# Kernel tuning notes

Measured on AMD Instinct MI355X. Metric: run time of the kernel, lower is better.

Reference implementation:

```python
import jax, jax.numpy as jnp
import numpy as np

IN_FEATURES = 512
HIDDEN_DIM = 512
B, S = 8, 2048


def setup_inputs() -> dict:
    key = jax.random.key(0)
    ks = jax.random.split(key, 7)
    sc_in = 1.0 / np.sqrt(IN_FEATURES)
    return {
        "x": jax.random.normal(ks[0], (B, S, IN_FEATURES), dtype=jnp.float32),
        "Wq": jax.random.normal(ks[1], (IN_FEATURES, HIDDEN_DIM), dtype=jnp.float32) * sc_in,
        "bq": jax.random.normal(ks[2], (HIDDEN_DIM,), dtype=jnp.float32) * 0.01,
        "Wk": jax.random.normal(ks[3], (IN_FEATURES, HIDDEN_DIM), dtype=jnp.float32) * sc_in,
        "bk": jax.random.normal(ks[4], (HIDDEN_DIM,), dtype=jnp.float32) * 0.01,
        "Wv": jax.random.normal(ks[5], (IN_FEATURES, HIDDEN_DIM), dtype=jnp.float32) * sc_in,
        "bv": jax.random.normal(ks[6], (HIDDEN_DIM,), dtype=jnp.float32) * 0.01,
    }


def reference(x, Wq, bq, Wk, bk, Wv, bv):
    # x: [B, S, in_features]
    q = jnp.einsum("bsf,fh->bsh", x, Wq) + bq  # [B, S, H]
    k = jnp.einsum("bsf,fh->bsh", x, Wk) + bk
    v = jnp.einsum("bsf,fh->bsh", x, Wv) + bv
    scale = 1.0 / jnp.sqrt(jnp.asarray(q.shape[-1], dtype=q.dtype))
    scores = jnp.einsum("bqh,bkh->bqk", q, k) * scale  # [B, S, S]
    weights = jax.nn.softmax(scores, axis=-1)
    return jnp.einsum("bqk,bkh->bqh", weights, v)  # [B, S, H]
```

## Files before the change

### kernel.cpp

```cpp
#include <hip/hip_runtime.h>
#include <hip/hip_bf16.h>

typedef __bf16 bf16;
typedef __bf16 bf16x8 __attribute__((ext_vector_type(8)));
typedef float  f32x4  __attribute__((ext_vector_type(4)));

#define MFMA16(a,b,c) __builtin_amdgcn_mfma_f32_16x16x32_bf16((a),(b),(c),0,0,0)

static const int BATCH = 8;
static const int SEQ   = 2048;
static const int HID   = 512;
static const int MTOT  = BATCH * SEQ;

__device__ __forceinline__ void gl2lds16(const void* g, void* l) {
    __builtin_amdgcn_global_load_lds(
        (const __attribute__((address_space(1))) void*)g,
        (__attribute__((address_space(3))) void*)l, 16, 0, 0);
}

__global__ void k_convert_x(const float* __restrict__ x, bf16* __restrict__ xb, int n4) {
    int i = blockIdx.x * blockDim.x + threadIdx.x;
    int stride = gridDim.x * blockDim.x;
    for (; i < n4; i += stride) {
        float4 v = ((const float4*)x)[i];
        union { bf16 h[4]; uint2 u; } o;
        o.h[0] = (bf16)v.x; o.h[1] = (bf16)v.y; o.h[2] = (bf16)v.z; o.h[3] = (bf16)v.w;
        ((uint2*)xb)[i] = o.u;
    }
}

__global__ void k_transpose_w(const float* __restrict__ Wq, const float* __restrict__ Wk,
                              const float* __restrict__ Wv, bf16* __restrict__ wt) {
    int z = blockIdx.z;
    const float* W = (z == 0) ? Wq : (z == 1) ? Wk : Wv;
    bf16* WT = wt + (size_t)z * HID * HID;
    __shared__ float tile[32][33];
    int t  = threadIdx.x;
    int tx = t & 31, ty = t >> 5;
    int f0 = blockIdx.y * 32, h0 = blockIdx.x * 32;
    for (int i = 0; i < 32; i += 8)
        tile[ty + i][tx] = W[(size_t)(f0 + ty + i) * HID + h0 + tx];
    __syncthreads();
    for (int i = 0; i < 32; i += 8)
        WT[(size_t)(h0 + ty + i) * HID + f0 + tx] = (bf16)tile[tx][ty + i];
}

__global__ __launch_bounds__(256) void
k_qkv(const bf16* __restrict__ xb, const bf16* __restrict__ wt,
      const float* __restrict__ bq, const float* __restrict__ bk, const float* __restrict__ bv,
      bf16* __restrict__ qb, bf16* __restrict__ kb, bf16* __restrict__ vt) {
    __shared__ __align__(16) char sm[65536];
    int z = blockIdx.z;
    const bf16*  WT   = wt + (size_t)z * HID * HID;
    const float* bias = (z == 0) ? bq : (z == 1) ? bk : bv;
    float scale = (z == 0) ? 0.044194173824159216f : 1.0f;

    int m0 = blockIdx.y * 128, n0 = blockIdx.x * 128;
    int t = threadIdx.x;
    int w = t >> 6, lane = t & 63, quad = lane >> 4, l15 = lane & 15;
    int wr = w >> 1, wc = w & 1;

    int rowA = t >> 3;
    int chS  = (t & 7) ^ (rowA & 7);
    const char* xga = (const char*)xb + ((size_t)(m0 + rowA) * 512 + chS * 8) * 2;
    const char* wga = (const char*)WT + ((size_t)(n0 + rowA) * 512 + chS * 8) * 2;

    const char* aK0 = sm + (wr * 64 + l15) * 128 + ((quad ^ (l15 & 7)) * 16);
    const char* aK1 = sm + (wr * 64 + l15) * 128 + (((4 + quad) ^ (l15 & 7)) * 16);
    const char* bK0 = sm + 16384 + (wc * 64 + l15) * 128 + ((quad ^ (l15 & 7)) * 16);
    const char* bK1 = sm + 16384 + (wc * 64 + l15) * 128 + (((4 + quad) ^ (l15 & 7)) * 16);

    f32x4 acc[4][4] = {};

#define QSTAGE(S)                                                             \
    {                                                                         \
        _Pragma("unroll")                                                     \
        for (int i = 0; i < 4; i++)                                           \
            gl2lds16(xga + i * 32768, sm + (S) * 32768 + i * 4096 + w * 1024);\
        _Pragma("unroll")                                                     \
        for (int i = 0; i < 4; i++)                                           \
            gl2lds16(wga + i * 32768,                                         \
                     sm + (S) * 32768 + 16384 + i * 4096 + w * 1024);         \
        xga += 128; wga += 128;                                               \
    }

#define QCOMP(CUR)                                                            \
    {                                                                         \
        bf16x8 af[4], bfr[4];                                                 \
        _Pragma("unroll")                                                     \
        for (int mt = 0; mt < 4; mt++)                                        \
            af[mt] = *(const bf16x8*)(aK0 + mt * 2048 + (CUR) * 32768);       \
        _Pragma("unroll")                                                     \
        for (int nt = 0; nt < 4; nt++)                                        \
            bfr[nt] = *(const bf16x8*)(bK0 + nt * 2048 + (CUR) * 32768);      \
        _Pragma("unroll")                                                     \
        for (int mt = 0; mt < 4; mt++)                                        \
            _Pragma("unroll")                                                 \
            for (int nt = 0; nt < 4; nt++)                                    \
                acc[mt][nt] = MFMA16(af[mt], bfr[nt], acc[mt][nt]);           \
        _Pragma("unroll")                                                     \
        for (int mt = 0; mt < 4; mt++)                                        \
            af[mt] = *(const bf16x8*)(aK1 + mt * 2048 + (CUR) * 32768);       \
        _Pragma("unroll")                                                     \
        for (int nt = 0; nt < 4; nt++)                                        \
            bfr[nt] = *(const bf16x8*)(bK1 + nt * 2048 + (CUR) * 32768);      \
        _Pragma("unroll")                                                     \
        for (int mt = 0; mt < 4; mt++)                                        \
            _Pragma("unroll")                                                 \
            for (int nt = 0; nt < 4; nt++)                                    \
                acc[mt][nt] = MFMA16(af[mt], bfr[nt], acc[mt][nt]);           \
    }

    QSTAGE(0);
    __syncthreads();
    for (int ii = 0; ii < 4; ii++) {
        QSTAGE(1);
        QCOMP(0);
        __syncthreads();
        if (ii < 3) QSTAGE(0);
        QCOMP(1);
        __syncthreads();
    }
#undef QSTAGE
#undef QCOMP

    if (z < 2) {
        bf16* out = (z == 0) ? qb : kb;
#pragma unroll
        for (int nt = 0; nt < 4; nt++) {
            int col = n0 + wc * 64 + nt * 16 + l15;
            float bc = bias[col];
#pragma unroll
            for (int mt = 0; mt < 4; mt++) {
                int rowb = m0 + wr * 64 + mt * 16 + quad * 4;
#pragma unroll
                for (int r = 0; r < 4; r++) {
                    float v = (acc[mt][nt][r] + bc) * scale;
                    out[(size_t)(rowb + r) * HID + col] = (bf16)v;
                }
            }
        }
    } else {
        bf16* st = (bf16*)sm;
#pragma unroll
        for (int nt = 0; nt < 4; nt++) {
            int colL = wc * 64 + nt * 16 + l15;
            float bc = bias[n0 + colL];
#pragma unroll
            for (int mt = 0; mt < 4; mt++) {
                int rowL = wr * 64 + mt * 16 + quad * 4;
#pragma unroll
                for (int r = 0; r < 4; r++)
                    st[(size_t)colL * 136 + rowL + r] = (bf16)(acc[mt][nt][r] + bc);
            }
        }
        __syncthreads();
        int b  = m0 >> 11;
        int s0 = m0 & 2047;
        bf16* vbase = vt + ((size_t)b * HID + n0) * SEQ + s0;
#pragma unroll
        for (int i = 0; i < 8; i++) {
            int p = i * 256 + t;
            int colL = p >> 4, ch = p & 15;
            *(uint4*)((char*)vbase + (size_t)colL * SEQ * 2 + ch * 16) =
                *(const uint4*)&st[(size_t)colL * 136 + ch * 8];
        }
    }
}

__global__ __launch_bounds__(512, 2) void
k_attn(const bf16* __restrict__ qb, const bf16* __restrict__ kbuf,
       const bf16* __restrict__ vt, float* __restrict__ out) {
    __shared__ __align__(16) char smem[76288];
    char* sm = smem;

    int j = blockIdx.x;
    int b = j & 7, qblk = j >> 3;
    int t = threadIdx.x, w = t >> 6, lane = t & 63, quad = lane >> 4, l15 = lane & 15;
    int rg = w & 3, kg = w >> 2;

    const bf16* Qrow   = qb + ((size_t)b * SEQ + qblk * 64 + rg * 16) * HID;
    const bf16* Kbase  = kbuf + (size_t)b * SEQ * HID;
    const bf16* VTbase = vt + (size_t)b * HID * SEQ;

    const char* kE = sm + (kg * 16 + l15) * 1024 + ((quad ^ (l15 & 7)) * 16);
    const char* kO = sm + (kg * 16 + l15) * 1024 + (((4 + quad) ^ (l15 & 7)) * 16);
    char*       pW = sm + 65536 + (rg * 16 + quad * 4) * 80 + (kg * 16 + l15) * 2;
    const char* pR = sm + 65536 + l15 * 80 + quad * 16;
    float*      mlx = (float*)(sm + 75776);

    const char* kgp = (const char*)Kbase + w * 1024 + ((lane ^ w) * 16);
    const char* vgp = (const char*)VTbase + (size_t)(w * 64 + l15) * 4096 + quad * 16;

    bf16x8 qf[16];
#pragma unroll
    for (int kt = 0; kt < 16; kt++)
        qf[kt] = *(const bf16x8*)&Qrow[(size_t)l15 * HID + kt * 32 + quad * 8];

    float l_acc[4] = {0.f, 0.f, 0.f, 0.f};
    f32x4 o_acc[16] = {};
    bf16x8 vf[2][4];

    const int NIT = SEQ / 32;

#define STAGE(S)                                                              \
    {                                                                         \
        _Pragma("unroll")                                                     \
        for (int jj = 0; jj < 4; jj++)                                        \
            gl2lds16(kgp + jj * 8192,                                         \
                     sm + (S) * 32768 + jj * 8192 + w * 1024);                \
        kgp += 32768;                                                         \
        __builtin_amdgcn_sched_barrier(0);                                    \
    }

#define VLOAD(VP)                                                             \
    {                                                                         \
        _Pragma("unroll")                                                     \
        for (int hs = 0; hs < 4; hs++)                                        \
            vf[VP][hs] = *(const bf16x8*)(vgp + hs * 65536);                  \
        vgp += 64;                                                            \
    }

#define QKP(CUR)                                                              \
    {                                                                         \
        f32x4 sa = {}, sb = {};                                               \
        __builtin_amdgcn_s_setprio(1);                                        \
        _Pragma("unroll")                                                     \
        for (int kp = 0; kp < 8; kp++) {                                      \
            bf16x8 kfe = *(const bf16x8*)(kE + kp * 128 + (CUR) * 32768);     \
            bf16x8 kfo = *(const bf16x8*)(kO + kp * 128 + (CUR) * 32768);     \
            sa = MFMA16(qf[2 * kp], kfe, sa);                                 \
            sb = MFMA16(qf[2 * kp + 1], kfo, sb);                             \
        }                                                                     \
        __builtin_amdgcn_s_setprio(0);                                        \
        _Pragma("unroll")                                                     \
        for (int r = 0; r < 4; r++) {                                         \
            float p = __expf(sa[r] + sb[r] - 8.0f);                           \
            l_acc[r] += p;                                                    \
            *(bf16*)(pW + (CUR) * 5120 + r * 80) = (bf16)p;                   \
        }                                                                     \
    }

#define PV(PB, VP)                                                            \
    {                                                                         \
        bf16x8 pa0 = *(const bf16x8*)(pR + (PB) * 5120 + 0 * 1280);           \
        bf16x8 pa1 = *(const bf16x8*)(pR + (PB) * 5120 + 1 * 1280);           \
        bf16x8 pa2 = *(const bf16x8*)(pR + (PB) * 5120 + 2 * 1280);           \
        bf16x8 pa3 = *(const bf16x8*)(pR + (PB) * 5120 + 3 * 1280);           \
        __builtin_amdgcn_s_setprio(1);                                        \
        _Pragma("unroll")                                                     \
        for (int hs = 0; hs < 4; hs++) {                                      \
            o_acc[0 * 4 + hs] = MFMA16(pa0, vf[VP][hs], o_acc[0 * 4 + hs]);   \
            o_acc[1 * 4 + hs] = MFMA16(pa1, vf[VP][hs], o_acc[1 * 4 + hs]);   \
            o_acc[2 * 4 + hs] = MFMA16(pa2, vf[VP][hs], o_acc[2 * 4 + hs]);   \
            o_acc[3 * 4 + hs] = MFMA16(pa3, vf[VP][hs], o_acc[3 * 4 + hs]);   \
        }                                                                     \
        __builtin_amdgcn_s_setprio(0);                                        \
    }

#define BAR()                                                                 \
    {                                                                         \
        asm volatile("s_waitcnt vmcnt(0) lgkmcnt(0)" ::: "memory");           \
        __builtin_amdgcn_sched_barrier(0);                                    \
        __builtin_amdgcn_s_barrier();                                         \
        __builtin_amdgcn_sched_barrier(0);                                    \
    }

    STAGE(0);

    BAR();
    STAGE(1);
    VLOAD(0);
    QKP(0);

    BAR();
    STAGE(0);
    VLOAD(1);
    PV(0, 0);
    QKP(1);

    for (int ii = 1; ii < NIT / 2; ii++) {
        BAR();
        STAGE(1);
        VLOAD(0);
        PV(1, 1);
        QKP(0);
        BAR();
        if (ii < NIT / 2 - 1) STAGE(0);
        VLOAD(1);
        PV(0, 0);
        QKP(1);
    }

    BAR();
    PV(1, 1);

    float lw[4];
#pragma unroll
    for (int r = 0; r < 4; r++) {
        float v = l_acc[r];
        for (int d = 1; d < 16; d <<= 1) v += __shfl_xor(v, d, 64);
        lw[r] = v;
    }
    __syncthreads();
    if (l15 == 0)
#pragma unroll
        for (int r = 0; r < 4; r++) mlx[kg * 64 + rg * 16 + quad * 4 + r] = lw[r];
    __syncthreads();

    float lt[4][4];
#pragma unroll
    for (int rgp = 0; rgp < 4; rgp++)
#pragma unroll
        for (int r = 0; r < 4; r++) {
            int row = rgp * 16 + quad * 4 + r;
            lt[rgp][r] = 1.0f / (mlx[row] + mlx[64 + row]);
        }
    float* obase = out + ((size_t)b * SEQ + qblk * 64) * HID + w * 64;
#pragma unroll
    for (int rgp = 0; rgp < 4; rgp++)
#pragma unroll
        for (int hs = 0; hs < 4; hs++)
#pragma unroll
            for (int r = 0; r < 4; r++)
                obase[(size_t)(rgp * 16 + quad * 4 + r) * HID + hs * 16 + l15] =
                    o_acc[rgp * 4 + hs][r] * lt[rgp][r];
#undef STAGE
#undef VLOAD
#undef QKP
#undef PV
#undef BAR
}

extern "C" void kernel_launch(void* const* d_in, const int* in_sizes, int n_in,
                              void* d_out, int out_size, void* d_ws, size_t ws_size,
                              hipStream_t stream) {
    const float* x  = (const float*)d_in[0];
    const float* Wq = (const float*)d_in[1];
    const float* bq = (const float*)d_in[2];
    const float* Wk = (const float*)d_in[3];
    const float* bk = (const float*)d_in[4];
    const float* Wv = (const float*)d_in[5];
    const float* bv = (const float*)d_in[6];
    float* out = (float*)d_out;

    char* ws = (char*)d_ws;
    const size_t SZ_XB = (size_t)MTOT * HID * 2;
    const size_t SZ_WT = (size_t)HID * HID * 2;
    bf16* xb = (bf16*)(ws);
    bf16* wt = (bf16*)(ws + SZ_XB);
    bf16* qb = (bf16*)(ws + SZ_XB + 3 * SZ_WT);
    bf16* kb = (bf16*)(ws + SZ_XB + 3 * SZ_WT + SZ_XB);
    bf16* vt = (bf16*)(ws + SZ_XB + 3 * SZ_WT + 2 * SZ_XB);

    k_convert_x<<<2048, 256, 0, stream>>>(x, xb, MTOT * HID / 4);
    k_transpose_w<<<dim3(16, 16, 3), 256, 0, stream>>>(Wq, Wk, Wv, wt);
    k_qkv<<<dim3(4, 128, 3), 256, 0, stream>>>(xb, wt, bq, bk, bv, qb, kb, vt);
    k_attn<<<256, 512, 0, stream>>>(qb, kb, vt, out);
}
```

Before: 249.8 us.

## Split attention key range across two blocks and add combine kernel

Templates the attention kernel on a key-split factor so that each (batch, query block) pair is handled by two workgroups, each covering half the keys. The partial unnormalized outputs and row sums go to the output buffer and a workspace buffer, and a new combine kernel sums them and normalizes. This doubles the grid from 256 to 512 blocks so more of the device's compute units are busy. The cost is an extra fp32 partial-output write and read plus one more kernel launch. The workspace is rearranged to fit the new buffers, and the code falls back to the single-pass path when the workspace is too small. The softmax appears to skip max subtraction, so adding partials directly is consistent. Launch bounds are also raised to 4 blocks per CU.

```diff
diff --git a/kernel.cpp b/kernel.cpp
--- a/kernel.cpp
+++ b/kernel.cpp
@@ -168,14 +168,17 @@
     }
 }
 
-__global__ __launch_bounds__(512, 2) void
+template <int NS>
+__global__ __launch_bounds__(512, 4) void
 k_attn(const bf16* __restrict__ qb, const bf16* __restrict__ kbuf,
-       const bf16* __restrict__ vt, float* __restrict__ out) {
+       const bf16* __restrict__ vt, float* __restrict__ out,
+       float* __restrict__ po1, float* __restrict__ pl) {
     __shared__ __align__(16) char smem[76288];
     char* sm = smem;
 
     int j = blockIdx.x;
-    int b = j & 7, qblk = j >> 3;
+    int b = j & 7, qblk = (j >> 3) & 31;
+    int ks = (NS == 2) ? (j >> 8) : 0;
     int t = threadIdx.x, w = t >> 6, lane = t & 63, quad = lane >> 4, l15 = lane & 15;
     int rg = w & 3, kg = w >> 2;
 
@@ -189,8 +192,10 @@
     const char* pR = sm + 65536 + l15 * 80 + quad * 16;
     float*      mlx = (float*)(sm + 75776);
 
-    const char* kgp = (const char*)Kbase + w * 1024 + ((lane ^ w) * 16);
-    const char* vgp = (const char*)VTbase + (size_t)(w * 64 + l15) * 4096 + quad * 16;
+    const char* kgp = (const char*)Kbase + (size_t)ks * 1024 * 1024
+                      + w * 1024 + ((lane ^ w) * 16);
+    const char* vgp = (const char*)VTbase + (size_t)(w * 64 + l15) * 4096
+                      + quad * 16 + ks * 2048;
 
     bf16x8 qf[16];
 #pragma unroll
@@ -201,7 +206,7 @@
     f32x4 o_acc[16] = {};
     bf16x8 vf[2][4];
 
-    const int NIT = SEQ / 32;
+    const int NIT = SEQ / 32 / NS;
 
 #define STAGE(S)                                                              \
     {                                                                         \
@@ -308,28 +313,61 @@
         for (int r = 0; r < 4; r++) mlx[kg * 64 + rg * 16 + quad * 4 + r] = lw[r];
     __syncthreads();
 
-    float lt[4][4];
-#pragma unroll
-    for (int rgp = 0; rgp < 4; rgp++)
-#pragma unroll
-        for (int r = 0; r < 4; r++) {
-            int row = rgp * 16 + quad * 4 + r;
-            lt[rgp][r] = 1.0f / (mlx[row] + mlx[64 + row]);
-        }
-    float* obase = out + ((size_t)b * SEQ + qblk * 64) * HID + w * 64;
-#pragma unroll
-    for (int rgp = 0; rgp < 4; rgp++)
-#pragma unroll
-        for (int hs = 0; hs < 4; hs++)
-#pragma unroll
-            for (int r = 0; r < 4; r++)
-                obase[(size_t)(rgp * 16 + quad * 4 + r) * HID + hs * 16 + l15] =
-                    o_acc[rgp * 4 + hs][r] * lt[rgp][r];
+    if constexpr (NS == 1) {
+        float lt[4][4];
+#pragma unroll
+        for (int rgp = 0; rgp < 4; rgp++)
+#pragma unroll
+            for (int r = 0; r < 4; r++) {
+                int row = rgp * 16 + quad * 4 + r;
+                lt[rgp][r] = 1.0f / (mlx[row] + mlx[64 + row]);
+            }
+        float* obase = out + ((size_t)b * SEQ + qblk * 64) * HID + w * 64;
+#pragma unroll
+        for (int rgp = 0; rgp < 4; rgp++)
+#pragma unroll
+            for (int hs = 0; hs < 4; hs++)
+#pragma unroll
+                for (int r = 0; r < 4; r++)
+                    obase[(size_t)(rgp * 16 + quad * 4 + r) * HID + hs * 16 + l15] =
+                        o_acc[rgp * 4 + hs][r] * lt[rgp][r];
+    } else {
+        if (t < 64)
+            pl[(size_t)ks * MTOT + (size_t)b * SEQ + qblk * 64 + t] =
+                mlx[t] + mlx[64 + t];
+        float* po = (ks == 0) ? out : po1;
+        float* obase = po + ((size_t)b * SEQ + qblk * 64) * HID + w * 64;
+#pragma unroll
+        for (int rgp = 0; rgp < 4; rgp++)
+#pragma unroll
+            for (int hs = 0; hs < 4; hs++)
+#pragma unroll
+                for (int r = 0; r < 4; r++)
+                    obase[(size_t)(rgp * 16 + quad * 4 + r) * HID + hs * 16 + l15] =
+                        o_acc[rgp * 4 + hs][r];
+    }
 #undef STAGE
 #undef VLOAD
 #undef QKP
 #undef PV
 #undef BAR
+}
+
+__global__ void k_combine(float* __restrict__ out, const float* __restrict__ po1,
+                          const float* __restrict__ pl, int nf4) {
+    int i = blockIdx.x * blockDim.x + threadIdx.x;
+    int stride = gridDim.x * blockDim.x;
+    for (; i < nf4; i += stride) {
+        int row = i >> 7;
+        float rr = 1.0f / (pl[row] + pl[MTOT + row]);
+        float4 a = ((const float4*)out)[i];
+        float4 c = ((const float4*)po1)[i];
+        a.x = (a.x + c.x) * rr;
+        a.y = (a.y + c.y) * rr;
+        a.z = (a.z + c.z) * rr;
+        a.w = (a.w + c.w) * rr;
+        ((float4*)out)[i] = a;
+    }
 }
 
 extern "C" void kernel_launch(void* const* d_in, const int* in_sizes, int n_in,
@@ -347,14 +385,23 @@
     char* ws = (char*)d_ws;
     const size_t SZ_XB = (size_t)MTOT * HID * 2;
     const size_t SZ_WT = (size_t)HID * HID * 2;
-    bf16* xb = (bf16*)(ws);
-    bf16* wt = (bf16*)(ws + SZ_XB);
-    bf16* qb = (bf16*)(ws + SZ_XB + 3 * SZ_WT);
-    bf16* kb = (bf16*)(ws + SZ_XB + 3 * SZ_WT + SZ_XB);
-    bf16* vt = (bf16*)(ws + SZ_XB + 3 * SZ_WT + 2 * SZ_XB);
+    const size_t SZ_O  = (size_t)MTOT * HID * 4;
+    bf16* qb = (bf16*)(ws);
+    bf16* kb = (bf16*)(ws + SZ_XB);
+    bf16* vt = (bf16*)(ws + 2 * SZ_XB);
+    bf16* xb = (bf16*)(ws + 3 * SZ_XB);
+    bf16* wt = (bf16*)(ws + 4 * SZ_XB);
+    float* po1 = (float*)(ws + 3 * SZ_XB);
+    float* pl  = (float*)(ws + 3 * SZ_XB + SZ_O);
+    const size_t NEED = 3 * SZ_XB + SZ_O + (size_t)2 * MTOT * 4;
 
     k_convert_x<<<2048, 256, 0, stream>>>(x, xb, MTOT * HID / 4);
     k_transpose_w<<<dim3(16, 16, 3), 256, 0, stream>>>(Wq, Wk, Wv, wt);
     k_qkv<<<dim3(4, 128, 3), 256, 0, stream>>>(xb, wt, bq, bk, bv, qb, kb, vt);
-    k_attn<<<256, 512, 0, stream>>>(qb, kb, vt, out);
-}
+    if (ws_size >= NEED) {
+        k_attn<2><<<512, 512, 0, stream>>>(qb, kb, vt, out, po1, pl);
+        k_combine<<<2048, 256, 0, stream>>>(out, po1, pl, MTOT * HID / 4);
+    } else {
+        k_attn<1><<<256, 512, 0, stream>>>(qb, kb, vt, out, nullptr, nullptr);
+    }
+}
```

New measurement: 893.3 us. +257.6%, slower.
